# Kernel tuning notes

Measured on AMD Instinct MI355X. Metric: run time of the kernel, lower is better.

Reference implementation:

```python
import jax, jax.numpy as jnp
import numpy as np

RHO = 1.0  # Lorentz curvature parameter


def setup_inputs() -> dict:
    key = jax.random.key(0)
    k1, k2, k3 = jax.random.split(key, 3)
    C, S, n, d = 512, 256, 16, 8  # cells, sites, states, hyperbolic dim
    # points on the Lorentz hyperboloid <x,x>_L = -RHO
    v = jax.random.normal(k1, (C, d), jnp.float32) * 0.5
    x0 = jnp.sqrt(RHO + jnp.sum(v * v, axis=-1, keepdims=True))
    X = jnp.concatenate([x0, v], axis=-1)  # [C, d+1]
    # per-site CTMC rate matrices: nonneg off-diagonal, rows sum to 0
    R = jax.random.uniform(k2, (S, n, n), jnp.float32) * 0.1
    R = R * (1.0 - jnp.eye(n, dtype=jnp.float32))
    Q = R - jnp.eye(n, dtype=jnp.float32) * jnp.sum(R, axis=-1)[..., None]
    char = jax.random.randint(k3, (C, S), 0, n).astype(jnp.int32)
    return {"X": X, "Q": Q, "char": char, "i": 0}


def _gather_last(A, idx):
    # A: [..., n], idx: [...] int -> A[..., idx] elementwise
    return jnp.take_along_axis(A, idx[..., None], axis=-1)[..., 0]


def reference(X, Q, char, i):
    C, S = char.shape
    n = Q.shape[-1]
    xi = X[i]
    # Lorentz (Minkowski) inner product and geodesic distance
    inner = -xi[0] * X[:, 0] + X[:, 1:] @ xi[1:]            # [C]
    u = jnp.maximum(-inner / RHO, 1.0 + 1e-6)
    dist = jnp.sqrt(RHO) * jnp.arccosh(u)                    # [C]
    t = 0.5 * dist
    # per-(cell j, site) transition probabilities P = expm(t_j * Q_site)
    M = t[:, None, None, None] * Q[None]                     # [C,S,n,n]
    P = jax.vmap(jax.scipy.linalg.expm)(M.reshape(-1, n, n)).reshape(C, S, n, n)
    s_i = char[i]                                            # [S]
    s_j = char                                               # [C,S]
    si_b = jnp.broadcast_to(s_i[None, :], (C, S))
    # ancestor a = 0 (unedited root state) is always feasible
    P0 = P[:, :, 0, :]                                       # [C,S,n]
    p0_si = _gather_last(P0, si_b)
    p0_sj = _gather_last(P0, s_j)
    # ancestor a = s is feasible iff s_i == s_j == s != 0 (irreversible edits)
    row_idx = jnp.broadcast_to(si_b[:, :, None, None], (C, S, 1, n))
    Prow = jnp.take_along_axis(P, row_idx, axis=2)[:, :, 0, :]  # P[c,s,s_i,:]
    ps_si = _gather_last(Prow, si_b)
    ps_sj = _gather_last(Prow, s_j)
    same = (si_b == s_j) & (si_b != 0)
    pi = 1.0 / n  # uniform stationary distribution
    cur = pi * (p0_si * p0_sj + jnp.where(same, ps_si * ps_sj, 0.0))  # [C,S]
    valid = jnp.arange(C) != i
    ll = jnp.where(valid[:, None], jnp.log(cur), 0.0)
    return jnp.sum(ll)
```

## Files before the change

kernel.cpp:

```cpp
#include <hip/hip_runtime.h>
#include <math.h>

#define C_N 512
#define S_N 256
#define NN  16
#define DP1 9
#define KT  24

__global__ __launch_bounds__(256) void site_kernel(
    const float* __restrict__ X, const float* __restrict__ Q,
    const int* __restrict__ ch, const int* __restrict__ ip,
    float* __restrict__ partials)
{
    const int s   = blockIdx.x;
    const int tid = threadIdx.x;

    __shared__ float w0[KT][NN];
    __shared__ float w1[KT][NN];
    __shared__ float lam_sh;
    __shared__ float red[4];

    const float* __restrict__ Qs = Q + s * NN * NN;
    const int i0 = ip[0];
    const int si = ch[i0 * S_N + s];

    if (tid < 32) {
        const int j = tid & 15;
        float dmax = -Qs[j * NN + j];
        #pragma unroll
        for (int off = 8; off; off >>= 1)
            dmax = fmaxf(dmax, __shfl_xor(dmax, off, 64));
        const float lam = dmax;
        if (tid == 0) lam_sh = lam;
        const float rl = 1.0f / lam;

        float a[NN];
        #pragma unroll
        for (int m = 0; m < NN; ++m)
            a[m] = Qs[m * NN + j] * rl + (m == j ? 1.0f : 0.0f);

        const int grp  = tid >> 4;
        const int base = grp << 4;
        float w = (grp == 0) ? (j == 0 ? 1.0f : 0.0f)
                             : (j == si ? 1.0f : 0.0f);
        if (grp == 0) w0[0][j] = w; else w1[0][j] = w;

        #pragma unroll
        for (int k = 1; k < KT; ++k) {
            float wn = 0.0f;
            #pragma unroll
            for (int m = 0; m < NN; ++m)
                wn = fmaf(__shfl(w, base + m, 64), a[m], wn);
            w = wn;
            if (grp == 0) w0[k][j] = w; else w1[k][j] = w;
        }
    }
    __syncthreads();

    const float lam = lam_sh;
    const float* __restrict__ xi = X + i0 * DP1;
    const float x0i = xi[0];
    float vi[8];
    #pragma unroll
    for (int d = 0; d < 8; ++d) vi[d] = xi[1 + d];

    float partial = 0.0f;
    #pragma unroll
    for (int cc = 0; cc < 2; ++cc) {
        const int c = tid + cc * 256;
        if (c == i0) continue;
        const float* __restrict__ xc = X + c * DP1;
        float inner = -x0i * xc[0];
        #pragma unroll
        for (int d = 0; d < 8; ++d) inner = fmaf(vi[d], xc[1 + d], inner);
        const float u = fmaxf(-inner, 1.0f + 1e-6f);
        const float dist = __logf(u + __fsqrt_rn(fmaf(u, u, -1.0f)));
        const float x = lam * (0.5f * dist);

        const int sj = ch[c * S_N + s];
        float p  = __expf(-x);
        float a0 = 0.f, a1 = 0.f, a2 = 0.f, a3 = 0.f;
        #pragma unroll
        for (int k = 0; k < KT; ++k) {
            a0 = fmaf(p, w0[k][si], a0);
            a1 = fmaf(p, w0[k][sj], a1);
            a2 = fmaf(p, w1[k][si], a2);
            a3 = fmaf(p, w1[k][sj], a3);
            p *= x * (1.0f / (float)(k + 1));
        }
        const bool same = (si == sj) && (si != 0);
        const float cur = 0.0625f * (a0 * a1 + (same ? a2 * a3 : 0.0f));
        partial += __logf(cur);
    }

    #pragma unroll
    for (int off = 32; off; off >>= 1)
        partial += __shfl_down(partial, off, 64);
    if ((tid & 63) == 0) red[tid >> 6] = partial;
    __syncthreads();
    if (tid == 0) partials[s] = red[0] + red[1] + red[2] + red[3];
}

__global__ __launch_bounds__(256) void reduce_kernel(
    const float* __restrict__ partials, float* __restrict__ out)
{
    const int tid = threadIdx.x;
    __shared__ float red[4];
    float v = partials[tid];
    #pragma unroll
    for (int off = 32; off; off >>= 1)
        v += __shfl_down(v, off, 64);
    if ((tid & 63) == 0) red[tid >> 6] = v;
    __syncthreads();
    if (tid == 0) out[0] = red[0] + red[1] + red[2] + red[3];
}

extern "C" void kernel_launch(void* const* d_in, const int* in_sizes, int n_in,
                              void* d_out, int out_size, void* d_ws, size_t ws_size,
                              hipStream_t stream) {
    const float* X  = (const float*)d_in[0];
    const float* Q  = (const float*)d_in[1];
    const int*   ch = (const int*)d_in[2];
    const int*   ip = (const int*)d_in[3];
    float* out      = (float*)d_out;
    float* partials = (float*)d_ws;

    site_kernel<<<S_N, 256, 0, stream>>>(X, Q, ch, ip, partials);
    reduce_kernel<<<1, 256, 0, stream>>>(partials, out);
}
```

Before: 14.34 us.

## Shorten uniformization series, split matvec across wave, transpose LDS for vector reads

Cuts the uniformization Taylor series from 24 to 16 terms. The serial 16x16 matvec chain is split across a full 64-lane wavefront, with 4 partial products per lane and a shuffle reduction, and the two chains run on two separate waves. Weight tables are stored transposed and padded so the per-cell loop can read float4 vectors from LDS. The distance computation is hoisted before the barrier so it overlaps with the matvec chain. Truncating the series risks accuracy for large t*lambda.

```diff
diff --git a/kernel.cpp b/kernel.cpp
--- a/kernel.cpp
+++ b/kernel.cpp
@@ -5,7 +5,8 @@
 #define S_N 256
 #define NN  16
 #define DP1 9
-#define KT  24
+#define KT  16
+#define KTP 20
 
 __global__ __launch_bounds__(256) void site_kernel(
     const float* __restrict__ X, const float* __restrict__ Q,
@@ -14,9 +15,10 @@
 {
     const int s   = blockIdx.x;
     const int tid = threadIdx.x;
+    const int wid = tid >> 6;
 
-    __shared__ float w0[KT][NN];
-    __shared__ float w1[KT][NN];
+    __shared__ __align__(16) float w0T[NN][KTP];
+    __shared__ __align__(16) float w1T[NN][KTP];
     __shared__ float lam_sh;
     __shared__ float red[4];
 
@@ -24,73 +26,95 @@
     const int i0 = ip[0];
     const int si = ch[i0 * S_N + s];
 
-    if (tid < 32) {
-        const int j = tid & 15;
+    if (wid < 2) {
+        const int lane = tid & 63;
+        const int j = lane & 15;
+        const int q = lane >> 4;
         float dmax = -Qs[j * NN + j];
         #pragma unroll
-        for (int off = 8; off; off >>= 1)
+        for (int off = 1; off < 16; off <<= 1)
             dmax = fmaxf(dmax, __shfl_xor(dmax, off, 64));
         const float lam = dmax;
         if (tid == 0) lam_sh = lam;
         const float rl = 1.0f / lam;
 
-        float a[NN];
+        float a[4];
         #pragma unroll
-        for (int m = 0; m < NN; ++m)
-            a[m] = Qs[m * NN + j] * rl + (m == j ? 1.0f : 0.0f);
+        for (int m = 0; m < 4; ++m) {
+            const int r = 4 * q + m;
+            a[m] = Qs[r * NN + j] * rl + (r == j ? 1.0f : 0.0f);
+        }
 
-        const int grp  = tid >> 4;
-        const int base = grp << 4;
-        float w = (grp == 0) ? (j == 0 ? 1.0f : 0.0f)
-                             : (j == si ? 1.0f : 0.0f);
-        if (grp == 0) w0[0][j] = w; else w1[0][j] = w;
+        float (*WT)[KTP] = (wid == 0) ? w0T : w1T;
+        const int tgt = (wid == 0) ? 0 : si;
+        float w = (j == tgt) ? 1.0f : 0.0f;
+        if (q == 0) WT[j][0] = w;
 
         #pragma unroll
         for (int k = 1; k < KT; ++k) {
-            float wn = 0.0f;
+            float acc = 0.0f;
             #pragma unroll
-            for (int m = 0; m < NN; ++m)
-                wn = fmaf(__shfl(w, base + m, 64), a[m], wn);
-            w = wn;
-            if (grp == 0) w0[k][j] = w; else w1[k][j] = w;
+            for (int m = 0; m < 4; ++m)
+                acc = fmaf(__shfl(w, 4 * q + m, 64), a[m], acc);
+            acc += __shfl_xor(acc, 16, 64);
+            acc += __shfl_xor(acc, 32, 64);
+            w = acc;
+            if (q == 0) WT[j][k] = w;
         }
     }
-    __syncthreads();
 
-    const float lam = lam_sh;
     const float* __restrict__ xi = X + i0 * DP1;
     const float x0i = xi[0];
     float vi[8];
     #pragma unroll
     for (int d = 0; d < 8; ++d) vi[d] = xi[1 + d];
 
-    float partial = 0.0f;
+    float x_c[2]; int sj_c[2]; bool ok_c[2];
     #pragma unroll
     for (int cc = 0; cc < 2; ++cc) {
         const int c = tid + cc * 256;
-        if (c == i0) continue;
+        ok_c[cc] = (c != i0);
         const float* __restrict__ xc = X + c * DP1;
         float inner = -x0i * xc[0];
         #pragma unroll
         for (int d = 0; d < 8; ++d) inner = fmaf(vi[d], xc[1 + d], inner);
         const float u = fmaxf(-inner, 1.0f + 1e-6f);
         const float dist = __logf(u + __fsqrt_rn(fmaf(u, u, -1.0f)));
-        const float x = lam * (0.5f * dist);
+        x_c[cc]  = 0.5f * dist;
+        sj_c[cc] = ch[c * S_N + s];
+    }
+    __syncthreads();
+    const float lam = lam_sh;
 
-        const int sj = ch[c * S_N + s];
-        float p  = __expf(-x);
+    float partial = 0.0f;
+    #pragma unroll
+    for (int cc = 0; cc < 2; ++cc) {
+        const float x  = lam * x_c[cc];
+        const int   sj = sj_c[cc];
+        const float4* __restrict__ u0p = (const float4*)&w0T[si][0];
+        const float4* __restrict__ u1p = (const float4*)&w0T[sj][0];
+        const float4* __restrict__ u2p = (const float4*)&w1T[si][0];
+        const float4* __restrict__ u3p = (const float4*)&w1T[sj][0];
+        float p = __expf(-x);
         float a0 = 0.f, a1 = 0.f, a2 = 0.f, a3 = 0.f;
         #pragma unroll
-        for (int k = 0; k < KT; ++k) {
-            a0 = fmaf(p, w0[k][si], a0);
-            a1 = fmaf(p, w0[k][sj], a1);
-            a2 = fmaf(p, w1[k][si], a2);
-            a3 = fmaf(p, w1[k][sj], a3);
-            p *= x * (1.0f / (float)(k + 1));
+        for (int kb = 0; kb < 4; ++kb) {
+            const float4 f0 = u0p[kb], f1 = u1p[kb], f2 = u2p[kb], f3 = u3p[kb];
+            #define STEP(K, CMP)                                   \
+                a0 = fmaf(p, f0.CMP, a0);                          \
+                a1 = fmaf(p, f1.CMP, a1);                          \
+                a2 = fmaf(p, f2.CMP, a2);                          \
+                a3 = fmaf(p, f3.CMP, a3);                          \
+                p *= x * (1.0f / (float)((K) + 1));
+            STEP(4 * kb + 0, x)
+            STEP(4 * kb + 1, y)
+            STEP(4 * kb + 2, z)
+            STEP(4 * kb + 3, w)
+            #undef STEP
         }
         const bool same = (si == sj) && (si != 0);
         const float cur = 0.0625f * (a0 * a1 + (same ? a2 * a3 : 0.0f));
-        partial += __logf(cur);
+        if (ok_c[cc]) partial += __logf(cur);
     }
 
     #pragma unroll
```

New measurement: 11.90 us. 17.0% less time.
